# Optimization experiments

Measured on AMD Instinct MI355X. Metric: run time of the kernel, lower is better.

## Reference

```python
import jax, jax.numpy as jnp
import numpy as np

B, L, D = 2, 2048, 2048
HEADS, DIM_HEAD = 16, 128
INNER = HEADS * DIM_HEAD
EPS = 1e-6


def _rmsnorm(x, w):
    # RMSNorm over last dim, matching nn.RMSNorm(inner_dim, eps)
    return x * jax.lax.rsqrt(jnp.mean(x * x, axis=-1, keepdims=True) + EPS) * w


def _rope_interleaved(x, cos, sin):
    # x: [B, L, INNER]; cos/sin: [1, L, INNER//2]
    x1 = x[..., 0::2]
    x2 = x[..., 1::2]
    o1 = x1 * cos - x2 * sin
    o2 = x1 * sin + x2 * cos
    return jnp.stack([o1, o2], axis=-1).reshape(x.shape)


def setup_inputs() -> dict:
    key = jax.random.key(0)
    ks = jax.random.split(key, 16)
    s = 0.02
    inp = {
        "x": jax.random.normal(ks[0], (B, L, D), jnp.float32),
        "pe_cos": jax.random.normal(ks[1], (1, L, INNER // 2), jnp.float32),
        "pe_sin": jax.random.normal(ks[2], (1, L, INNER // 2), jnp.float32),
        "logit_log_scale": jax.random.uniform(ks[3], (1, L, 1), jnp.float32),
        "wq": jax.random.normal(ks[4], (D, INNER), jnp.float32) * s,
        "bq": jnp.zeros((INNER,), jnp.float32),
        "wk": jax.random.normal(ks[5], (D, INNER), jnp.float32) * s,
        "bk": jnp.zeros((INNER,), jnp.float32),
        "wv": jax.random.normal(ks[6], (D, INNER), jnp.float32) * s,
        "bv": jnp.zeros((INNER,), jnp.float32),
        "qn_w": jnp.ones((INNER,), jnp.float32),
        "kn_w": jnp.ones((INNER,), jnp.float32),
        "wo": jax.random.normal(ks[7], (INNER, D), jnp.float32) * s,
        "bo": jnp.zeros((D,), jnp.float32),
    }
    return inp


def reference(x, pe_cos, pe_sin, logit_log_scale, wq, bq, wk, bk, wv, bv, qn_w, kn_w, wo, bo):
    # QKV projections
    q = _rmsnorm(x @ wq + bq, qn_w)
    k = _rmsnorm(x @ wk + bk, kn_w)
    v = x @ wv + bv
    # Interleaved RoPE on flattened inner dim
    q = _rope_interleaved(q, pe_cos, pe_sin)
    k = _rope_interleaved(k, pe_cos, pe_sin)
    # Position-dependent logit temperature applied to Q
    q = q * logit_log_scale
    # Split heads: [B, L, H, Dh]
    q = q.reshape(B, L, HEADS, DIM_HEAD)
    k = k.reshape(B, L, HEADS, DIM_HEAD)
    v = v.reshape(B, L, HEADS, DIM_HEAD)
    scale = 1.0 / jnp.sqrt(jnp.asarray(DIM_HEAD, jnp.float32))
    scores = jnp.einsum("bqhd,bkhd->bhqk", q, k) * scale  # [B, H, L, L]
    causal = jnp.tril(jnp.ones((L, L), bool))
    scores = jnp.where(causal[None, None], scores, jnp.asarray(-1e30, scores.dtype))
    attn = jax.nn.softmax(scores, axis=-1)
    out = jnp.einsum("bhqk,bkhd->bqhd", attn, v).reshape(B, L, INNER)
    return out @ wo + bo
```

## Files before the change

kernel.cpp:

```cpp
#include <hip/hip_runtime.h>
#include <hip/hip_bf16.h>

typedef __bf16 bf16x8_t __attribute__((ext_vector_type(8)));
typedef float  f32x4_t  __attribute__((ext_vector_type(4)));

#define B_     2
#define L_     2048
#define D_     2048
#define H_     16
#define DH_    128
#define INNER_ 2048
#define M_     (B_ * L_)

__device__ __forceinline__ void gld_lds16(const void* g, void* l) {
    __builtin_amdgcn_global_load_lds(
        (const __attribute__((address_space(1))) void*)g,
        (__attribute__((address_space(3))) void*)l,
        16, 0, 0);
}

__device__ __forceinline__ unsigned short f2bf(float f) {
    __hip_bfloat16 h = __float2bfloat16(f);
    return *(unsigned short*)&h;
}
__device__ __forceinline__ float bf2f(unsigned short s) {
    return __uint_as_float(((unsigned)s) << 16);
}

__global__ __launch_bounds__(256)
void k_cast(const float* __restrict__ in, unsigned short* __restrict__ out) {
    const size_t i = ((size_t)blockIdx.x * 256 + threadIdx.x) * 4;
    float4 v = *(const float4*)(in + i);
    ushort4 o;
    o.x = f2bf(v.x); o.y = f2bf(v.y); o.z = f2bf(v.z); o.w = f2bf(v.w);
    *(ushort4*)(out + i) = o;
}

__global__ __launch_bounds__(256)
void k_transpose_cast(const float* __restrict__ in, unsigned short* __restrict__ out) {
    __shared__ unsigned short tile[32][33];
    const int t  = threadIdx.x;
    const int r  = t >> 3;
    const int c4 = (t & 7) << 2;
    const size_t ib = ((size_t)blockIdx.y * 32 + r) * 2048 + blockIdx.x * 32 + c4;
    float4 v = *(const float4*)(in + ib);
    tile[r][c4 + 0] = f2bf(v.x); tile[r][c4 + 1] = f2bf(v.y);
    tile[r][c4 + 2] = f2bf(v.z); tile[r][c4 + 3] = f2bf(v.w);
    __syncthreads();
    ushort4 o;
    o.x = tile[c4 + 0][r]; o.y = tile[c4 + 1][r];
    o.z = tile[c4 + 2][r]; o.w = tile[c4 + 3][r];
    const size_t ob = ((size_t)blockIdx.x * 32 + r) * 2048 + blockIdx.y * 32 + c4;
    *(ushort4*)(out + ob) = o;
}

__global__ __launch_bounds__(256)
void k_transpose2048(const unsigned short* __restrict__ in,
                     unsigned short* __restrict__ out) {
    __shared__ unsigned short tile[32][33];
    const int t  = threadIdx.x;
    const int r  = t >> 3;
    const int c4 = (t & 7) << 2;
    const size_t ib = ((size_t)blockIdx.y * 32 + r) * 2048 + blockIdx.x * 32 + c4;
    ushort4 v = *(const ushort4*)(in + ib);
    tile[r][c4 + 0] = v.x; tile[r][c4 + 1] = v.y;
    tile[r][c4 + 2] = v.z; tile[r][c4 + 3] = v.w;
    __syncthreads();
    ushort4 o;
    o.x = tile[c4 + 0][r]; o.y = tile[c4 + 1][r];
    o.z = tile[c4 + 2][r]; o.w = tile[c4 + 3][r];
    const size_t ob = ((size_t)blockIdx.x * 32 + r) * 2048 + blockIdx.y * 32 + c4;
    *(ushort4*)(out + ob) = o;
}

#define GEMM_BODY(A_, Bt_, K_)                                                 \
    __shared__ __align__(16) __hip_bfloat16 As[128 * 32];                      \
    __shared__ __align__(16) __hip_bfloat16 Bs[128 * 32];                      \
    const int t    = threadIdx.x;                                              \
    const int lane = t & 63;                                                   \
    const int wave = t >> 6;                                                   \
    const int quad = lane >> 4;                                                \
    const int l16  = lane & 15;                                                \
    const int wm   = (wave >> 1) * 64;                                         \
    const int wn   = (wave & 1) * 64;                                          \
    const int srow = t >> 2;                                                   \
    const int scol = (t & 3) << 3;                                             \
    const __hip_bfloat16* Ag = A_  + (size_t)(tileM + srow) * K_ + scol;       \
    const __hip_bfloat16* Bg = Bt_ + (size_t)(tileN + srow) * K_ + scol;       \
    __hip_bfloat16* Asl  = &As[t * 8];                                         \
    __hip_bfloat16* Asl2 = &As[2048 + t * 8];                                  \
    __hip_bfloat16* Bsl  = &Bs[t * 8];                                         \
    __hip_bfloat16* Bsl2 = &Bs[2048 + t * 8];                                  \
    const size_t rowskip = (size_t)64 * K_;                                    \
    f32x4_t acc[4][4];                                                         \
    _Pragma("unroll") for (int i = 0; i < 4; i++)                              \
        _Pragma("unroll") for (int j = 0; j < 4; j++)                          \
            acc[i][j] = (f32x4_t){0.f, 0.f, 0.f, 0.f};                         \
    for (int k0 = 0; k0 < K_; k0 += 32) {                                      \
        __syncthreads();                                                       \
        gld_lds16(Ag + k0,           Asl);                                     \
        gld_lds16(Ag + rowskip + k0, Asl2);                                    \
        gld_lds16(Bg + k0,           Bsl);                                     \
        gld_lds16(Bg + rowskip + k0, Bsl2);                                    \
        __syncthreads();                                                       \
        bf16x8_t af[4], bfr[4];                                                \
        _Pragma("unroll") for (int i = 0; i < 4; i++)                          \
            af[i] = *(const bf16x8_t*)&As[(wm + i * 16 + l16) * 32 + quad * 8];\
        _Pragma("unroll") for (int j = 0; j < 4; j++)                          \
            bfr[j] = *(const bf16x8_t*)&Bs[(wn + j * 16 + l16) * 32 + quad * 8];\
        _Pragma("unroll") for (int i = 0; i < 4; i++)                          \
            _Pragma("unroll") for (int j = 0; j < 4; j++)                      \
                acc[i][j] = __builtin_amdgcn_mfma_f32_16x16x32_bf16(           \
                    af[i], bfr[j], acc[i][j], 0, 0, 0);                        \
    }

__global__ __launch_bounds__(256)
void k_gemm_bt_f32(const __hip_bfloat16* __restrict__ A,
                   const __hip_bfloat16* __restrict__ Bt,
                   const float* __restrict__ bias,
                   float* __restrict__ C,
                   int M, int N, int K) {
    const int tileM = blockIdx.x * 128;
    const int tileN = blockIdx.y * 128;
    GEMM_BODY(A, Bt, K)
#pragma unroll
    for (int i = 0; i < 4; i++)
#pragma unroll
        for (int r = 0; r < 4; r++) {
            const int m = tileM + wm + i * 16 + quad * 4 + r;
#pragma unroll
            for (int j = 0; j < 4; j++) {
                const int n = tileN + wn + j * 16 + l16;
                C[(size_t)m * N + n] = acc[i][j][r] + bias[n];
            }
        }
}

__global__ __launch_bounds__(256)
void k_gemm_qkv(const __hip_bfloat16* __restrict__ A,
                const __hip_bfloat16* __restrict__ Bt,
                const float* __restrict__ bq, const float* __restrict__ bk,
                const float* __restrict__ bv,
                __hip_bfloat16* __restrict__ qo, __hip_bfloat16* __restrict__ ko,
                __hip_bfloat16* __restrict__ vo) {
    const int tileM = blockIdx.x * 128;
    const int tileN = blockIdx.y * 128;
    GEMM_BODY(A, Bt, D_)
    const int sel  = blockIdx.y >> 4;
    const int nbas = tileN - sel * INNER_;
    const float* bias = (sel == 0) ? bq : (sel == 1) ? bk : bv;
    __hip_bfloat16* C = (sel == 0) ? qo : (sel == 1) ? ko : vo;
#pragma unroll
    for (int i = 0; i < 4; i++)
#pragma unroll
        for (int r = 0; r < 4; r++) {
            const int m = tileM + wm + i * 16 + quad * 4 + r;
#pragma unroll
            for (int j = 0; j < 4; j++) {
                const int n = nbas + wn + j * 16 + l16;
                C[(size_t)m * INNER_ + n] = __float2bfloat16(acc[i][j][r] + bias[n]);
            }
        }
}

__global__ __launch_bounds__(256)
void k_rmsrope(__hip_bfloat16* __restrict__ buf,
               const float* __restrict__ w,
               const float* __restrict__ pcos,
               const float* __restrict__ psin,
               const float* __restrict__ lls,
               float extra) {
    const int row = blockIdx.x;
    const int l   = row & (L_ - 1);
    const int t   = threadIdx.x;
    __hip_bfloat16* p = buf + (size_t)row * INNER_ + t * 8;

    float x[8];
    {
        const unsigned short* ps = (const unsigned short*)p;
        ushort4 a = *(const ushort4*)ps;
        ushort4 b = *(const ushort4*)(ps + 4);
        unsigned short s[8] = {a.x, a.y, a.z, a.w, b.x, b.y, b.z, b.w};
#pragma unroll
        for (int i = 0; i < 8; i++) x[i] = bf2f(s[i]);
    }
    float ss = 0.f;
#pragma unroll
    for (int i = 0; i < 8; i++) ss += x[i] * x[i];
#pragma unroll
    for (int off = 32; off >= 1; off >>= 1) ss += __shfl_down(ss, off);
    __shared__ float red[4];
    if ((t & 63) == 0) red[t >> 6] = ss;
    __syncthreads();
    ss = red[0] + red[1] + red[2] + red[3];
    const float rstd = rsqrtf(ss * (1.0f / (float)INNER_) + 1e-6f);

    float scale = extra;
    if (lls) scale *= lls[l];

    const float4 c4 = ((const float4*)(pcos + (size_t)l * (INNER_ / 2)))[t];
    const float4 s4 = ((const float4*)(psin + (size_t)l * (INNER_ / 2)))[t];
    const float cc[4] = {c4.x, c4.y, c4.z, c4.w};
    const float sn[4] = {s4.x, s4.y, s4.z, s4.w};
    const float4 w0 = ((const float4*)w)[t * 2];
    const float4 w1 = ((const float4*)w)[t * 2 + 1];
    const float ww[8] = {w0.x, w0.y, w0.z, w0.w, w1.x, w1.y, w1.z, w1.w};

    union { __hip_bfloat16 h[8]; uint4 u; } pk;
#pragma unroll
    for (int pi = 0; pi < 4; pi++) {
        const float y1 = x[pi * 2]     * rstd * ww[pi * 2];
        const float y2 = x[pi * 2 + 1] * rstd * ww[pi * 2 + 1];
        pk.h[pi * 2]     = __float2bfloat16((y1 * cc[pi] - y2 * sn[pi]) * scale);
        pk.h[pi * 2 + 1] = __float2bfloat16((y1 * sn[pi] + y2 * cc[pi]) * scale);
    }
    *(uint4*)p = pk.u;
}

__global__ __launch_bounds__(256)
void k_attn(const __hip_bfloat16* __restrict__ q,
            const __hip_bfloat16* __restrict__ k,
            const __hip_bfloat16* __restrict__ vT,
            __hip_bfloat16* __restrict__ o) {
    __shared__ __align__(16) __hip_bfloat16 Ks[64 * 128];
    __shared__ __align__(16) __hip_bfloat16 Vs[128 * 64];
    __shared__ __align__(16) __hip_bfloat16 Pt[8][16 * 72];

    const int p  = blockIdx.x;
    const int bh = blockIdx.y;
    const int b  = bh >> 4;
    const int h  = bh & 15;
    const int t = threadIdx.x, wave = t >> 6, lane = t & 63;
    const int quad = lane >> 4, l16 = lane & 15;

    const int krow = t >> 4, kcol = ((t & 15) ^ krow) << 3;
    const int vrow = t >> 3, vcol = ((t & 7) ^ (vrow & 7)) << 3;

    for (int half = 0; half < 2; ++half) {
        const int qt = half ? (15 - p) : p;
        const int rowbase = qt * 128 + wave * 32;

        bf16x8_t aq[2][4];
#pragma unroll
        for (int s = 0; s < 2; s++) {
            const size_t qoff = (size_t)(b * L_ + rowbase + s * 16 + l16) * INNER_ + h * DH_;
#pragma unroll
            for (int kk = 0; kk < 4; kk++)
                aq[s][kk] = *(const bf16x8_t*)(q + qoff + kk * 32 + quad * 8);
        }

        f32x4_t oacc[2][8];
#pragma unroll
        for (int s = 0; s < 2; s++)
#pragma unroll
            for (int jj = 0; jj < 8; jj++) oacc[s][jj] = (f32x4_t){0.f, 0.f, 0.f, 0.f};
        float m_[2] = {-1e30f, -1e30f};
        float l_[2] = {0.f, 0.f};

        const int nkt = 2 * qt + 2;
        for (int kt = 0; kt < nkt; ++kt) {
            const int kv0 = kt * 64;
            __syncthreads();
#pragma unroll
            for (int i = 0; i < 4; i++) {
                gld_lds16(k  + (size_t)(b * L_ + kv0 + i * 16 + krow) * INNER_ + h * DH_ + kcol,
                          &Ks[t * 8 + i * 2048]);
                gld_lds16(vT + ((size_t)bh * DH_ + i * 32 + vrow) * L_ + kv0 + vcol,
                          &Vs[t * 8 + i * 2048]);
            }
            __syncthreads();

            if (kv0 > rowbase + 31) continue;

            f32x4_t sacc[2][4];
#pragma unroll
            for (int s = 0; s < 2; s++)
#pragma unroll
                for (int tt = 0; tt < 4; tt++) sacc[s][tt] = (f32x4_t){0.f, 0.f, 0.f, 0.f};
#pragma unroll
            for (int kk = 0; kk < 4; kk++) {
                bf16x8_t kf[4];
#pragma unroll
                for (int tt = 0; tt < 4; tt++)
                    kf[tt] = *(const bf16x8_t*)&Ks[(tt * 16 + l16) * 128 + (((kk * 4 + quad) ^ l16) << 3)];
#pragma unroll
                for (int s = 0; s < 2; s++)
#pragma unroll
                    for (int tt = 0; tt < 4; tt++)
                        sacc[s][tt] = __builtin_amdgcn_mfma_f32_16x16x32_bf16(
                            kf[tt], aq[s][kk], sacc[s][tt], 0, 0, 0);
            }

            const bool diag = (kv0 + 63 > rowbase);
#pragma unroll
            for (int s = 0; s < 2; s++) {
                const int sbase = rowbase + s * 16;
                if (diag) {
                    const int qrow = sbase + l16;
#pragma unroll
                    for (int tt = 0; tt < 4; tt++)
#pragma unroll
                        for (int r = 0; r < 4; r++)
                            if (kv0 + tt * 16 + quad * 4 + r > qrow) sacc[s][tt][r] = -1e30f;
                }
                float mx = sacc[s][0][0];
#pragma unroll
                for (int tt = 0; tt < 4; tt++)
#pragma unroll
                    for (int r = 0; r < 4; r++) mx = fmaxf(mx, sacc[s][tt][r]);
                mx = fmaxf(mx, __shfl_xor(mx, 16));
                mx = fmaxf(mx, __shfl_xor(mx, 32));
                const float mnew = fmaxf(m_[s], mx);
                const float alpha = exp2f(m_[s] - mnew);
                m_[s] = mnew;

                float ls = 0.f;
#pragma unroll
                for (int tt = 0; tt < 4; tt++) {
                    ushort4 pk;
                    float p0 = exp2f(sacc[s][tt][0] - mnew);
                    float p1 = exp2f(sacc[s][tt][1] - mnew);
                    float p2 = exp2f(sacc[s][tt][2] - mnew);
                    float p3 = exp2f(sacc[s][tt][3] - mnew);
                    ls += (p0 + p1) + (p2 + p3);
                    pk.x = f2bf(p0); pk.y = f2bf(p1); pk.z = f2bf(p2); pk.w = f2bf(p3);
                    *(ushort4*)&Pt[wave * 2 + s][l16 * 72 + tt * 16 + quad * 4] = pk;
                }
                ls += __shfl_xor(ls, 16);
                ls += __shfl_xor(ls, 32);
                l_[s] = l_[s] * alpha + ls;
#pragma unroll
                for (int jj = 0; jj < 8; jj++) {
                    oacc[s][jj][0] *= alpha; oacc[s][jj][1] *= alpha;
                    oacc[s][jj][2] *= alpha; oacc[s][jj][3] *= alpha;
                }
            }

#pragma unroll
            for (int kk2 = 0; kk2 < 2; kk2++) {
                bf16x8_t pf0 = *(const bf16x8_t*)&Pt[wave * 2 + 0][l16 * 72 + kk2 * 32 + quad * 8];
                bf16x8_t pf1 = *(const bf16x8_t*)&Pt[wave * 2 + 1][l16 * 72 + kk2 * 32 + quad * 8];
#pragma unroll
                for (int jj = 0; jj < 8; jj++) {
                    bf16x8_t vf = *(const bf16x8_t*)
                        &Vs[(jj * 16 + l16) * 64 + (((kk2 * 4 + quad) ^ (l16 & 7)) << 3)];
                    oacc[0][jj] = __builtin_amdgcn_mfma_f32_16x16x32_bf16(vf, pf0, oacc[0][jj], 0, 0, 0);
                    oacc[1][jj] = __builtin_amdgcn_mfma_f32_16x16x32_bf16(vf, pf1, oacc[1][jj], 0, 0, 0);
                }
            }
        }

#pragma unroll
        for (int s = 0; s < 2; s++) {
            const float inv = 1.0f / l_[s];
            __hip_bfloat16* orow = o + (size_t)(b * L_ + rowbase + s * 16 + l16) * INNER_ + h * DH_;
#pragma unroll
            for (int jj = 0; jj < 8; jj++) {
                ushort4 pk;
                pk.x = f2bf(oacc[s][jj][0] * inv);
                pk.y = f2bf(oacc[s][jj][1] * inv);
                pk.z = f2bf(oacc[s][jj][2] * inv);
                pk.w = f2bf(oacc[s][jj][3] * inv);
                *(ushort4*)(orow + jj * 16 + quad * 4) = pk;
            }
        }
    }
}

extern "C" void kernel_launch(void* const* d_in, const int* in_sizes, int n_in,
                              void* d_out, int out_size, void* d_ws, size_t ws_size,
                              hipStream_t stream) {
    const float* x      = (const float*)d_in[0];
    const float* pe_cos = (const float*)d_in[1];
    const float* pe_sin = (const float*)d_in[2];
    const float* lls    = (const float*)d_in[3];
    const float* wq     = (const float*)d_in[4];
    const float* bq     = (const float*)d_in[5];
    const float* wk     = (const float*)d_in[6];
    const float* bk     = (const float*)d_in[7];
    const float* wv     = (const float*)d_in[8];
    const float* bv     = (const float*)d_in[9];
    const float* qn     = (const float*)d_in[10];
    const float* kn     = (const float*)d_in[11];
    const float* wo     = (const float*)d_in[12];
    const float* bo     = (const float*)d_in[13];

    char* ws = (char*)d_ws;
    const size_t SZ_W = (size_t)D_ * INNER_ * 2;
    const size_t SZ_M = (size_t)M_ * INNER_ * 2;
    __hip_bfloat16* xb     = (__hip_bfloat16*)ws;  ws += SZ_M;
    __hip_bfloat16* wqkvT  = (__hip_bfloat16*)ws;  ws += 3 * SZ_W;
    __hip_bfloat16* woT    = (__hip_bfloat16*)ws;  ws += SZ_W;
    __hip_bfloat16* qb     = (__hip_bfloat16*)ws;  ws += SZ_M;
    __hip_bfloat16* kb     = (__hip_bfloat16*)ws;  ws += SZ_M;
    __hip_bfloat16* vb     = (__hip_bfloat16*)ws;  ws += SZ_M;
    __hip_bfloat16* vT     = (__hip_bfloat16*)ws;  ws += SZ_M;
    __hip_bfloat16* ab     = (__hip_bfloat16*)ws;  ws += SZ_M;
    (void)in_sizes; (void)n_in; (void)out_size; (void)ws_size;

    const dim3 tb(256);
    const dim3 gT(64, 64);

    k_cast<<<(M_ * D_) / 1024, tb, 0, stream>>>(x, (unsigned short*)xb);

    k_transpose_cast<<<gT, tb, 0, stream>>>(wq, (unsigned short*)(wqkvT));
    k_transpose_cast<<<gT, tb, 0, stream>>>(wk, (unsigned short*)(wqkvT + (size_t)INNER_ * D_));
    k_transpose_cast<<<gT, tb, 0, stream>>>(wv, (unsigned short*)(wqkvT + 2 * (size_t)INNER_ * D_));
    k_transpose_cast<<<gT, tb, 0, stream>>>(wo, (unsigned short*)woT);

    k_gemm_qkv<<<dim3(M_ / 128, 48), tb, 0, stream>>>(xb, wqkvT, bq, bk, bv, qb, kb, vb);

    const float qextra = 0.08838834764831843f  * 1.4426950408889634f ;
    k_rmsrope<<<M_, tb, 0, stream>>>(qb, qn, pe_cos, pe_sin, lls, qextra);
    k_rmsrope<<<M_, tb, 0, stream>>>(kb, kn, pe_cos, pe_sin, nullptr, 1.0f);

    k_transpose2048<<<gT, tb, 0, stream>>>((const unsigned short*)vb, (unsigned short*)vT);
    k_transpose2048<<<gT, tb, 0, stream>>>((const unsigned short*)(vb + (size_t)L_ * INNER_),
                                           (unsigned short*)(vT + (size_t)L_ * INNER_));

    k_attn<<<dim3(8, B_ * H_), tb, 0, stream>>>(qb, kb, vT, ab);

    k_gemm_bt_f32<<<dim3(M_ / 128, D_ / 128), tb, 0, stream>>>(ab, woT, bo, (float*)d_out, M_, D_, INNER_);
}
```

Before: 458.7 us.

## Fuse weight casts, write V transposed from GEMM, merge rmsrope, widen attention blocks

Merges the four weight transpose-cast launches into one 3D-grid launch and merges the Q and K rmsnorm/rope launches into one. The QKV GEMM epilogue now writes V directly in per-head transposed layout, which removes the separate V buffer and its two transpose kernels. The attention kernel moves to 512 threads with 8 waves, each owning 16 query rows instead of 32. That gives more waves per block but halves the MFMA work per K/V tile load per wave, and the V stores from the GEMM become strided.

```diff
diff --git a/kernel.cpp b/kernel.cpp
--- a/kernel.cpp
+++ b/kernel.cpp
@@ -37,7 +37,13 @@
 }
 
 __global__ __launch_bounds__(256)
-void k_transpose_cast(const float* __restrict__ in, unsigned short* __restrict__ out) {
+void k_wtrans4(const float* __restrict__ w0, const float* __restrict__ w1,
+               const float* __restrict__ w2, const float* __restrict__ w3,
+               unsigned short* __restrict__ d0, unsigned short* __restrict__ d1,
+               unsigned short* __restrict__ d2, unsigned short* __restrict__ d3) {
+    const int z = blockIdx.z;
+    const float* in = (z == 0) ? w0 : (z == 1) ? w1 : (z == 2) ? w2 : w3;
+    unsigned short* out = (z == 0) ? d0 : (z == 1) ? d1 : (z == 2) ? d2 : d3;
     __shared__ unsigned short tile[32][33];
     const int t  = threadIdx.x;
     const int r  = t >> 3;
@@ -46,25 +52,6 @@
     float4 v = *(const float4*)(in + ib);
     tile[r][c4 + 0] = f2bf(v.x); tile[r][c4 + 1] = f2bf(v.y);
     tile[r][c4 + 2] = f2bf(v.z); tile[r][c4 + 3] = f2bf(v.w);
-    __syncthreads();
-    ushort4 o;
-    o.x = tile[c4 + 0][r]; o.y = tile[c4 + 1][r];
-    o.z = tile[c4 + 2][r]; o.w = tile[c4 + 3][r];
-    const size_t ob = ((size_t)blockIdx.x * 32 + r) * 2048 + blockIdx.y * 32 + c4;
-    *(ushort4*)(out + ob) = o;
-}
-
-__global__ __launch_bounds__(256)
-void k_transpose2048(const unsigned short* __restrict__ in,
-                     unsigned short* __restrict__ out) {
-    __shared__ unsigned short tile[32][33];
-    const int t  = threadIdx.x;
-    const int r  = t >> 3;
-    const int c4 = (t & 7) << 2;
-    const size_t ib = ((size_t)blockIdx.y * 32 + r) * 2048 + blockIdx.x * 32 + c4;
-    ushort4 v = *(const ushort4*)(in + ib);
-    tile[r][c4 + 0] = v.x; tile[r][c4 + 1] = v.y;
-    tile[r][c4 + 2] = v.z; tile[r][c4 + 3] = v.w;
     __syncthreads();
     ushort4 o;
     o.x = tile[c4 + 0][r]; o.y = tile[c4 + 1][r];
@@ -142,34 +129,55 @@
                 const float* __restrict__ bq, const float* __restrict__ bk,
                 const float* __restrict__ bv,
                 __hip_bfloat16* __restrict__ qo, __hip_bfloat16* __restrict__ ko,
-                __hip_bfloat16* __restrict__ vo) {
+                __hip_bfloat16* __restrict__ vTo) {
     const int tileM = blockIdx.x * 128;
     const int tileN = blockIdx.y * 128;
     GEMM_BODY(A, Bt, D_)
     const int sel  = blockIdx.y >> 4;
     const int nbas = tileN - sel * INNER_;
-    const float* bias = (sel == 0) ? bq : (sel == 1) ? bk : bv;
-    __hip_bfloat16* C = (sel == 0) ? qo : (sel == 1) ? ko : vo;
-#pragma unroll
-    for (int i = 0; i < 4; i++)
-#pragma unroll
-        for (int r = 0; r < 4; r++) {
-            const int m = tileM + wm + i * 16 + quad * 4 + r;
+    if (sel < 2) {
+        const float* bias = (sel == 0) ? bq : bk;
+        __hip_bfloat16* C = (sel == 0) ? qo : ko;
+#pragma unroll
+        for (int i = 0; i < 4; i++)
+#pragma unroll
+            for (int r = 0; r < 4; r++) {
+                const int m = tileM + wm + i * 16 + quad * 4 + r;
+#pragma unroll
+                for (int j = 0; j < 4; j++) {
+                    const int n = nbas + wn + j * 16 + l16;
+                    C[(size_t)m * INNER_ + n] = __float2bfloat16(acc[i][j][r] + bias[n]);
+                }
+            }
+    } else {
+        const int bb = tileM >> 11;
+#pragma unroll
+        for (int i = 0; i < 4; i++) {
+            const int l0 = (tileM + wm + i * 16 + quad * 4) & (L_ - 1);
 #pragma unroll
             for (int j = 0; j < 4; j++) {
-                const int n = nbas + wn + j * 16 + l16;
-                C[(size_t)m * INNER_ + n] = __float2bfloat16(acc[i][j][r] + bias[n]);
+                const int n  = nbas + wn + j * 16 + l16;
+                const int hh = n >> 7, dd = n & 127;
+                const float bvn = bv[n];
+                ushort4 pk;
+                pk.x = f2bf(acc[i][j][0] + bvn);
+                pk.y = f2bf(acc[i][j][1] + bvn);
+                pk.z = f2bf(acc[i][j][2] + bvn);
+                pk.w = f2bf(acc[i][j][3] + bvn);
+                *(ushort4*)(vTo + ((size_t)(bb * H_ + hh) * DH_ + dd) * L_ + l0) = pk;
             }
         }
+    }
 }
 
 __global__ __launch_bounds__(256)
-void k_rmsrope(__hip_bfloat16* __restrict__ buf,
-               const float* __restrict__ w,
-               const float* __restrict__ pcos,
-               const float* __restrict__ psin,
-               const float* __restrict__ lls,
-               float extra) {
+void k_rmsrope2(__hip_bfloat16* __restrict__ qb, __hip_bfloat16* __restrict__ kb,
+                const float* __restrict__ qn, const float* __restrict__ kn,
+                const float* __restrict__ pcos, const float* __restrict__ psin,
+                const float* __restrict__ lls, float qextra) {
+    const int which = blockIdx.y;
+    __hip_bfloat16* buf = which ? kb : qb;
+    const float* w = which ? kn : qn;
     const int row = blockIdx.x;
     const int l   = row & (L_ - 1);
     const int t   = threadIdx.x;
@@ -195,8 +203,7 @@
     ss = red[0] + red[1] + red[2] + red[3];
     const float rstd = rsqrtf(ss * (1.0f / (float)INNER_) + 1e-6f);
 
-    float scale = extra;
-    if (lls) scale *= lls[l];
+    const float scale = which ? 1.0f : (qextra * lls[l]);
 
     const float4 c4 = ((const float4*)(pcos + (size_t)l * (INNER_ / 2)))[t];
     const float4 s4 = ((const float4*)(psin + (size_t)l * (INNER_ / 2)))[t];
@@ -217,7 +224,7 @@
     *(uint4*)p = pk.u;
 }
 
-__global__ __launch_bounds__(256)
+__global__ __launch_bounds__(512)
 void k_attn(const __hip_bfloat16* __restrict__ q,
             const __hip_bfloat16* __restrict__ k,
             const __hip_bfloat16* __restrict__ vT,
@@ -233,50 +240,45 @@
     const int t = threadIdx.x, wave = t >> 6, lane = t & 63;
     const int quad = lane >> 4, l16 = lane & 15;
 
-    const int krow = t >> 4, kcol = ((t & 15) ^ krow) << 3;
-    const int vrow = t >> 3, vcol = ((t & 7) ^ (vrow & 7)) << 3;
+    const int kr = t >> 4;
+    const int kc = ((t & 15) ^ (kr & 15)) << 3;
+    const int vr = t >> 3;
+    const int vc = ((t & 7) ^ (vr & 7)) << 3;
+    const __hip_bfloat16* kbase = k  + (size_t)b * L_ * INNER_ + h * DH_;
+    const __hip_bfloat16* vbase = vT + (size_t)bh * DH_ * L_;
 
     for (int half = 0; half < 2; ++half) {
         const int qt = half ? (15 - p) : p;
-        const int rowbase = qt * 128 + wave * 32;
-
-        bf16x8_t aq[2][4];
-#pragma unroll
-        for (int s = 0; s < 2; s++) {
-            const size_t qoff = (size_t)(b * L_ + rowbase + s * 16 + l16) * INNER_ + h * DH_;
+        const int rowbase = qt * 128 + wave * 16;
+
+        bf16x8_t aq[4];
+        {
+            const size_t qoff = (size_t)(b * L_ + rowbase + l16) * INNER_ + h * DH_;
 #pragma unroll
             for (int kk = 0; kk < 4; kk++)
-                aq[s][kk] = *(const bf16x8_t*)(q + qoff + kk * 32 + quad * 8);
+                aq[kk] = *(const bf16x8_t*)(q + qoff + kk * 32 + quad * 8);
         }
 
-        f32x4_t oacc[2][8];
-#pragma unroll
-        for (int s = 0; s < 2; s++)
-#pragma unroll
-            for (int jj = 0; jj < 8; jj++) oacc[s][jj] = (f32x4_t){0.f, 0.f, 0.f, 0.f};
-        float m_[2] = {-1e30f, -1e30f};
-        float l_[2] = {0.f, 0.f};
+        f32x4_t oacc[8];
+#pragma unroll
+        for (int jj = 0; jj < 8; jj++) oacc[jj] = (f32x4_t){0.f, 0.f, 0.f, 0.f};
+        float m_ = -1e30f, l_ = 0.f;
 
         const int nkt = 2 * qt + 2;
         for (int kt = 0; kt < nkt; ++kt) {
             const int kv0 = kt * 64;
             __syncthreads();
-#pragma unroll
-            for (int i = 0; i < 4; i++) {
-                gld_lds16(k  + (size_t)(b * L_ + kv0 + i * 16 + krow) * INNER_ + h * DH_ + kcol,
-                          &Ks[t * 8 + i * 2048]);
-                gld_lds16(vT + ((size_t)bh * DH_ + i * 32 + vrow) * L_ + kv0 + vcol,
-                          &Vs[t * 8 + i * 2048]);
-            }
+            gld_lds16(kbase + (size_t)(kv0 + kr)      * INNER_ + kc, &Ks[t * 8]);
+            gld_lds16(kbase + (size_t)(kv0 + 32 + kr) * INNER_ + kc, &Ks[4096 + t * 8]);
+            gld_lds16(vbase + (size_t)vr        * L_ + kv0 + vc, &Vs[t * 8]);
+            gld_lds16(vbase + (size_t)(64 + vr) * L_ + kv0 + vc, &Vs[4096 + t * 8]);
             __syncthreads();
 
-            if (kv0 > rowbase + 31) continue;
-
-            f32x4_t sacc[2][4];
-#pragma unroll
-            for (int s = 0; s < 2; s++)
-#pragma unroll
-                for (int tt = 0; tt < 4; tt++) sacc[s][tt] = (f32x4_t){0.f, 0.f, 0.f, 0.f};
+            if (kv0 > rowbase + 15) continue;
+
+            f32x4_t sacc[4];
+#pragma unroll
+            for (int tt = 0; tt < 4; tt++) sacc[tt] = (f32x4_t){0.f, 0.f, 0.f, 0.f};
 #pragma unroll
             for (int kk = 0; kk < 4; kk++) {
                 bf16x8_t kf[4];
@@ -284,83 +286,74 @@
                 for (int tt = 0; tt < 4; tt++)
                     kf[tt] = *(const bf16x8_t*)&Ks[(tt * 16 + l16) * 128 + (((kk * 4 + quad) ^ l16) << 3)];
 #pragma unroll
-                for (int s = 0; s < 2; s++)
-#pragma unroll
-                    for (int tt = 0; tt < 4; tt++)
-                        sacc[s][tt] = __builtin_amdgcn_mfma_f32_16x16x32_bf16(
-                            kf[tt], aq[s][kk], sacc[s][tt], 0, 0, 0);
-            }
-
-            const bool diag = (kv0 + 63 > rowbase);
-#pragma unroll
-            for (int s = 0; s < 2; s++) {
-                const int sbase = rowbase + s * 16;
-                if (diag) {
-                    const int qrow = sbase + l16;
-#pragma unroll
-                    for (int tt = 0; tt < 4; tt++)
-#pragma unroll
-                        for (int r = 0; r < 4; r++)
-                            if (kv0 + tt * 16 + quad * 4 + r > qrow) sacc[s][tt][r] = -1e30f;
-                }
-                float mx = sacc[s][0][0];
-#pragma unroll
                 for (int tt = 0; tt < 4; tt++)
-#pragma unroll
-                    for (int r = 0; r < 4; r++) mx = fmaxf(mx, sacc[s][tt][r]);
-                mx = fmaxf(mx, __shfl_xor(mx, 16));
-                mx = fmaxf(mx, __shfl_xor(mx, 32));
-                const float mnew = fmaxf(m_[s], mx);
-                const float alpha = exp2f(m_[s] - mnew);
-                m_[s] = mnew;
-
-                float ls = 0.f;
-#pragma unroll
-                for (int tt = 0; tt < 4; tt++) {
-                    ushort4 pk;
-                    float p0 = exp2f(sacc[s][tt][0] - mnew);
-                    float p1 = exp2f(sacc[s][tt][1] - mnew);
-                    float p2 = exp2f(sacc[s][tt][2] - mnew);
-                    float p3 = exp2f(sacc[s][tt][3] - mnew);
-                    ls += (p0 + p1) + (p2 + p3);
-                    pk.x = f2bf(p0); pk.y = f2bf(p1); pk.z = f2bf(p2); pk.w = f2bf(p3);
-                    *(ushort4*)&Pt[wave * 2 + s][l16 * 72 + tt * 16 + quad * 4] = pk;
-                }
-                ls += __shfl_xor(ls, 16);
-                ls += __shfl_xor(ls, 32);
-                l_[s] = l_[s] * alpha + ls;
-#pragma unroll
-                for (int jj = 0; jj < 8; jj++) {
-                    oacc[s][jj][0] *= alpha; oacc[s][jj][1] *= alpha;
-                    oacc[s][jj][2] *= alpha; oacc[s][jj][3] *= alpha;
-                }
+                    sacc[tt] = __builtin_amdgcn_mfma_f32_16x16x32_bf16(
+                        kf[tt], aq[kk], sacc[tt], 0, 0, 0);
+            }
+
+            if (kv0 + 63 > rowbase) {
+                const int qrow = rowbase + l16;
+#pragma unroll
+                for (int tt = 0; tt < 4; tt++)
+#pragma unroll
+                    for (int r = 0; r < 4; r++)
+                        if (kv0 + tt * 16 + quad * 4 + r > qrow) sacc[tt][r] = -1e30f;
+            }
+
+            float mx = sacc[0][0];
+#pragma unroll
+            for (int tt = 0; tt < 4; tt++)
+#pragma unroll
+                for (int r = 0; r < 4; r++) mx = fmaxf(mx, sacc[tt][r]);
+            mx = fmaxf(mx, __shfl_xor(mx, 16));
+            mx = fmaxf(mx, __shfl_xor(mx, 32));
+            const float mnew = fmaxf(m_, mx);
+            const float alpha = exp2f(m_ - mnew);
+            m_ = mnew;
+
+            float ls = 0.f;
+#pragma unroll
+            for (int tt = 0; tt < 4; tt++) {
+                ushort4 pk;
+                float p0 = exp2f(sacc[tt][0] - mnew);
+                float p1 = exp2f(sacc[tt][1] - mnew);
+                float p2 = exp2f(sacc[tt][2] - mnew);
+                float p3 = exp2f(sacc[tt][3] - mnew);
+                ls += (p0 + p1) + (p2 + p3);
+                pk.x = f2bf(p0); pk.y = f2bf(p1); pk.z = f2bf(p2); pk.w = f2bf(p3);
+                *(ushort4*)&Pt[wave][l16 * 72 + tt * 16 + quad * 4] = pk;
+            }
+            ls += __shfl_xor(ls, 16);
+            ls += __shfl_xor(ls, 32);
+            l_ = l_ * alpha + ls;
+#pragma unroll
+            for (int jj = 0; jj < 8; jj++) {
+                oacc[jj][0] *= alpha; oacc[jj][1] *= alpha;
+                oacc[jj][2] *= alpha; oacc[jj][3] *= alpha;
             }
 
 #pragma unroll
             for (int kk2 = 0; kk2 < 2; kk2++) {
-                bf16x8_t pf0 = *(const bf16x8_t*)&Pt[wave * 2 + 0][l16 * 72 + kk2 * 32 + quad * 8];
-                bf16x8_t pf1 = *(const bf16x8_t*)&Pt[wave * 2 + 1][l16 * 72 + kk2 * 32 + quad * 8];
+                bf16x8_t pf = *(const bf16x8_t*)&Pt[wave][l16 * 72 + kk2 * 32 + quad * 8];
 #pragma unroll
                 for (int jj = 0; jj < 8; jj++) {
                     bf16x8_t vf = *(const bf16x8_t*)
                         &Vs[(jj * 16 + l16) * 64 + (((kk2 * 4 + quad) ^ (l16 & 7)) << 3)];
-                    oacc[0][jj] = __builtin_amdgcn_mfma_f32_16x16x32_bf16(vf, pf0, oacc[0][jj], 0, 0, 0);
-                    oacc[1][jj] = __builtin_amdgcn_mfma_f32_16x16x32_bf16(vf, pf1, oacc[1][jj], 0, 0, 0);
+                    oacc[jj] = __builtin_amdgcn_mfma_f32_16x16x32_bf16(vf, pf, oacc[jj], 0, 0, 0);
                 }
             }
         }
 
-#pragma unroll
-        for (int s = 0; s < 2; s++) {
-            const float inv = 1.0f / l_[s];
-            __hip_bfloat16* orow = o + (size_t)(b * L_ + rowbase + s * 16 + l16) * INNER_ + h * DH_;
+        {
+            const float inv = 1.0f / l_;
+            __hip_bfloat16* orow = o + (size_t)(b * L_ + rowbase + l16) * INNER_ + h * DH_;
 #pragma unroll
             for (int jj = 0; jj < 8; jj++) {
                 ushort4 pk;
-                pk.x = f2bf(oacc[s][jj][0] * inv);
-                pk.y = f2bf(oacc[s][jj][1] * inv);
-                pk.z = f2bf(oacc[s][jj][2] * inv);
-                pk.w = f2bf(oacc[s][jj][3] * inv);
+                pk.x = f2bf(oacc[jj][0] * inv);
+                pk.y = f2bf(oacc[jj][1] * inv);
+                pk.z = f2bf(oacc[jj][2] * inv);
+                pk.w = f2bf(oacc[jj][3] * inv);
                 *(ushort4*)(orow + jj * 16 + quad * 4) = pk;
             }
         }
@@ -393,32 +386,27 @@
     __hip_bfloat16* woT    = (__hip_bfloat16*)ws;  ws += SZ_W;
     __hip_bfloat16* qb     = (__hip_bfloat16*)ws;  ws += SZ_M;
     __hip_bfloat16* kb     = (__hip_bfloat16*)ws;  ws += SZ_M;
-    __hip_bfloat16* vb     = (__hip_bfloat16*)ws;  ws += SZ_M;
     __hip_bfloat16* vT     = (__hip_bfloat16*)ws;  ws += SZ_M;
     __hip_bfloat16* ab     = (__hip_bfloat16*)ws;  ws += SZ_M;
     (void)in_sizes; (void)n_in; (void)out_size; (void)ws_size;
 
     const dim3 tb(256);
-    const dim3 gT(64, 64);
 
     k_cast<<<(M_ * D_) / 1024, tb, 0, stream>>>(x, (unsigned short*)xb);
 
-    k_transpose_cast<<<gT, tb, 0, stream>>>(wq, (unsigned short*)(wqkvT));
-    k_transpose_cast<<<gT, tb, 0, stream>>>(wk, (unsigned short*)(wqkvT + (size_t)INNER_ * D_));
-    k_transpose_cast<<<gT, tb, 0, stream>>>(wv, (unsigned short*)(wqkvT + 2 * (size_t)INNER_ * D_));
-    k_transpose_cast<<<gT, tb, 0, stream>>>(wo, (unsigned short*)woT);
-
-    k_gemm_qkv<<<dim3(M_ / 128, 48), tb, 0, stream>>>(xb, wqkvT, bq, bk, bv, qb, kb, vb);
+    k_wtrans4<<<dim3(64, 64, 4), tb, 0, stream>>>(
+        wq, wk, wv, wo,
+        (unsigned short*)wqkvT,
+        (unsigned short*)(wqkvT + (size_t)INNER_ * D_),
+        (unsigned short*)(wqkvT + 2 * (size_t)INNER_ * D_),
+        (unsigned short*)woT);
+
+    k_gemm_qkv<<<dim3(M_ / 128, 48), tb, 0, stream>>>(xb, wqkvT, bq, bk, bv, qb, kb, vT);
 
     const float qextra = 0.08838834764831843f  * 1.4426950408889634f ;
-    k_rmsrope<<<M_, tb, 0, stream>>>(qb, qn, pe_cos, pe_sin, lls, qextra);
-    k_rmsrope<<<M_, tb, 0, stream>>>(kb, kn, pe_cos, pe_sin, nullptr, 1.0f);
-
-    k_transpose2048<<<gT, tb, 0, stream>>>((const unsigned short*)vb, (unsigned short*)vT);
-    k_transpose2048<<<gT, tb, 0, stream>>>((const unsigned short*)(vb + (size_t)L_ * INNER_),
-                                           (unsigned short*)(vT + (size_t)L_ * INNER_));
-
-    k_attn<<<dim3(8, B_ * H_), tb, 0, stream>>>(qb, kb, vT, ab);
+    k_rmsrope2<<<dim3(M_, 2), tb, 0, stream>>>(qb, kb, qn, kn, pe_cos, pe_sin, lls, qextra);
+
+    k_attn<<<dim3(8, B_ * H_), dim3(512), 0, stream>>>(qb, kb, vT, ab);
 
     k_gemm_bt_f32<<<dim3(M_ / 128, D_ / 128), tb, 0, stream>>>(ab, woT, bo, (float*)d_out, M_, D_, INNER_);
 }
```

Result: faster. 446.9 us (-2.6%).
